# Performance work log

Hardware: AMD Instinct MI355X
Metric: run time of the kernel (lower is better)

The kernel has to match this reference:

```python
import jax, jax.numpy as jnp
import numpy as np

B = 4_000_000

# physical constants from initBatteryParams
R_ = 8.3144621
F_ = 96487.0
ALPHA = 0.5
SN = 0.0002
SP = 0.0002
KN = 20000.0
KP = 20000.0
VOL = 2.2e-05
VOLS = 0.1 * VOL
VOLB = VOL - VOLS
TO = 10.0
TSN = 90.0
TSP = 90.0
U0P = 4.03
U0N = 0.01
QMAX_BASE = 10000.0
RO_BASE = 10.0
T_DIFFUSION = 7.0e6  # repo default; attribute used in getNextState
DT = 1.0


def setup_inputs() -> dict:
    key = jax.random.key(0)
    ks = jax.random.split(key, 12)
    qMax = 1.4 * jnp.ones((B,), jnp.float32)   # 14000/qMaxBASE
    Ro = 0.015 * jnp.ones((B,), jnp.float32)   # 0.15/RoBASE
    # physically plausible initial state (get_initial_state) + small noise
    qM = qMax * QMAX_BASE  # [B]
    Tb = 292.1 + 0.5 * jax.random.normal(ks[0], (B, 1), jnp.float32)
    Vo = 0.01 * jax.random.uniform(ks[1], (B, 1), jnp.float32)
    Vsn = 0.01 * jax.random.uniform(ks[2], (B, 1), jnp.float32)
    Vsp = 0.01 * jax.random.uniform(ks[3], (B, 1), jnp.float32)
    jitter = lambda k: 1.0 + 0.01 * jax.random.normal(k, (B, 1), jnp.float32)
    qnB = (qM * 0.6 * VOLB / VOL)[:, None] * jitter(ks[4])
    qnS = (qM * 0.6 * VOLS / VOL)[:, None] * jitter(ks[5])
    qpB = (qM * 0.4 * VOLB / VOL)[:, None] * jitter(ks[6])
    qpS = (qM * 0.4 * VOLS / VOL)[:, None] * jitter(ks[7])
    states = jnp.concatenate([Tb, Vo, Vsn, Vsp, qnB, qnS, qpB, qpS], axis=1)
    inputs = 1.0 + 2.0 * jax.random.uniform(ks[8], (B, 1), jnp.float32)  # current [A]
    kw = jax.random.split(ks[9], 8)
    return {
        "inputs": inputs, "states": states, "qMax": qMax, "Ro": Ro,
        "Wp0": 0.5 * jax.random.normal(kw[0], (8, 1), jnp.float32),
        "bp0": 0.1 * jax.random.normal(kw[1], (8,), jnp.float32),
        "Wp2": 0.5 * jax.random.normal(kw[2], (4, 8), jnp.float32),
        "bp2": 0.1 * jax.random.normal(kw[3], (4,), jnp.float32),
        "Wp4": 0.5 * jax.random.normal(kw[4], (1, 4), jnp.float32),
        "bp4": 0.1 * jax.random.normal(kw[5], (1,), jnp.float32),
        "Wn": 0.0016 * jnp.ones((1, 1), jnp.float32),  # ~fitted Linear(1,1)
        "bn": -0.0008 * jnp.ones((1,), jnp.float32),
    }


def _mlp_p(x, Wp0, bp0, Wp2, bp2, Wp4, bp4):
    h = jnp.tanh(x @ Wp0.T + bp0)
    h = jnp.tanh(h @ Wp2.T + bp2)
    return h @ Wp4.T + bp4


def _cell(inputs, states, qMax, Ro, Wp0, bp0, Wp2, bp2, Wp4, bp4, Wn, bn):
    Tb, Vo, Vsn, Vsp, qnB, qnS, qpB, qpS = jnp.split(states, 8, axis=1)
    i = inputs  # [B,1]
    qSMax = (qMax * QMAX_BASE * VOLS / VOL)[:, None]  # [B,1]
    # --- getNextState ---
    xpS = jnp.clip(qpS / qSMax, 1e-18, 1.0)
    xnS = jnp.clip(qnS / qSMax, 1e-18, 1.0)
    Jn0 = 1e-18 + KN * (1.0 - xnS) ** ALPHA * xnS ** ALPHA
    Jp0 = 1e-18 + KP * (1.0 - xpS) ** ALPHA * xpS ** ALPHA
    qdotDiffusionBSn = (qnB / VOLB - qnS / VOLS) / T_DIFFUSION
    qdotDiffusionBSp = (qpB / VOLB - qpS / VOLS) / T_DIFFUSION
    Jn = i / SN
    Jp = i / SP
    VoNominal = i * Ro[:, None] * RO_BASE
    VsnNominal = R_ * Tb / F_ / ALPHA * jnp.arcsinh(Jn / (2.0 * Jn0))
    VspNominal = R_ * Tb / F_ / ALPHA * jnp.arcsinh(Jp / (2.0 * Jp0))
    Tb2 = Tb  # Tbdot = 0
    Vo2 = Vo + (VoNominal - Vo) / TO * DT
    Vsn2 = Vsn + (VsnNominal - Vsn) / TSN * DT
    Vsp2 = Vsp + (VspNominal - Vsp) / TSP * DT
    qnB2 = qnB + (-qdotDiffusionBSn) * DT
    qnS2 = qnS + (qdotDiffusionBSn - i) * DT
    qpB2 = qpB + (-qdotDiffusionBSp) * DT
    qpS2 = qpS + (i + qdotDiffusionBSp) * DT
    XNew = jnp.concatenate([Tb2, Vo2, Vsn2, Vsp2, qnB2, qnS2, qpB2, qpS2], axis=1)
    # --- getNextOutput (on XNew) ---
    xpS_o = qpS2 / qSMax
    xnS_o = qnS2 / qSMax
    VepMLP = _mlp_p(xpS_o, Wp0, bp0, Wp2, bp2, Wp4, bp4)
    VenMLP = xnS_o @ Wn.T + bn
    safe_log_p = jnp.clip((1.0 - xpS_o) / xpS_o, 1e-18, 1e18)
    safe_log_n = jnp.clip((1.0 - xnS_o) / xnS_o, 1e-18, 1e18)
    Vep = U0P + R_ * Tb2 / F_ * jnp.log(safe_log_p) + VepMLP
    Ven = U0N + R_ * Tb2 / F_ * jnp.log(safe_log_n) + VenMLP
    V = Vep - Ven - Vo2 - Vsn2 - Vsp2
    return V, XNew


def reference(inputs, states, qMax, Ro, Wp0, bp0, Wp2, bp2, Wp4, bp4, Wn, bn):
    return _cell(inputs, states, qMax, Ro, Wp0, bp0, Wp2, bp2, Wp4, bp4, Wn, bn)
```

## Files before the change

### kernel.cpp

```cpp
#include <hip/hip_runtime.h>
#include <math.h>

typedef float v4f __attribute__((ext_vector_type(4)));
typedef float v2f __attribute__((ext_vector_type(2)));

#define RTF       (8.3144621f / 96487.0f)
#define VOLS_     2.2e-06f
#define VOLB_     1.98e-05f
#define INV_TDIFF (1.0f / 7.0e6f)

#define LUT_N 4096

__device__ __forceinline__ float fdiv_fast(float a, float b) {
    return __fdividef(a, b);
}

__device__ __forceinline__ float asinh_pos(float x) {
    return __logf(x + sqrtf(fmaf(x, x, 1.0f)));
}

__global__ __launch_bounds__(256) void build_lut_kernel(
    const float* __restrict__ Wp0, const float* __restrict__ bp0,
    const float* __restrict__ Wp2, const float* __restrict__ bp2,
    const float* __restrict__ Wp4, const float* __restrict__ bp4,
    float* __restrict__ lutJ, v2f* __restrict__ lutO)
{
    int idx = blockIdx.x * blockDim.x + threadIdx.x;
    if (idx >= LUT_N) return;
    float x = (float)idx * (1.0f / (float)(LUT_N - 1));

    float j0 = 1e-18f + 20000.0f * sqrtf(fmaxf(x * (1.0f - x), 0.0f));
    lutJ[idx] = 1.0f / (2.0f * j0);

    float h1[8];
#pragma unroll
    for (int j = 0; j < 8; j++)
        h1[j] = tanhf(fmaf(x, Wp0[j], bp0[j]));
    float mlp = bp4[0];
#pragma unroll
    for (int k = 0; k < 4; k++) {
        float a = bp2[k];
#pragma unroll
        for (int j = 0; j < 8; j++)
            a = fmaf(h1[j], Wp2[k * 8 + j], a);
        mlp = fmaf(tanhf(a), Wp4[k], mlp);
    }

    float r = fminf(fmaxf((1.0f - x) / fmaxf(x, 1e-30f), 1e-18f), 1e18f);
    float lg = RTF * logf(r);

    v2f o; o.x = mlp; o.y = lg;
    lutO[idx] = o;
}

__global__ __launch_bounds__(256) void battery_cell_kernel(
    const float* __restrict__ inp,
    const float* __restrict__ st,
    const float* __restrict__ qMaxp,
    const float* __restrict__ Rop,
    const float* __restrict__ Wn,
    const float* __restrict__ bn,
    const float* __restrict__ lutJ,
    const v2f*   __restrict__ lutO,
    float* __restrict__ outV,
    float* __restrict__ outX,
    int B)
{
    int b = blockIdx.x * blockDim.x + threadIdx.x;
    if (b >= B) return;

    const v4f* st4 = (const v4f*)st;
    v4f s0 = st4[2 * b];
    v4f s1 = st4[2 * b + 1];
    float Tb  = s0.x, Vo  = s0.y, Vsn = s0.z, Vsp = s0.w;
    float qnB = s1.x, qnS = s1.y, qpB = s1.z, qpS = s1.w;
    float i   = inp[b];
    float qm  = qMaxp[b];
    float ro  = Rop[b];
    float wn  = Wn[0], wbn = bn[0];

    float invq = fdiv_fast(1.0f, qm * 1000.0f);

    float xpS = fminf(fmaxf(qpS * invq, 1e-18f), 1.0f);
    float xnS = fminf(fmaxf(qnS * invq, 1e-18f), 1.0f);

    float tn = xnS * (float)(LUT_N - 1);
    float tp = xpS * (float)(LUT_N - 1);
    int in0 = min((int)tn, LUT_N - 2);
    int ip0 = min((int)tp, LUT_N - 2);
    float fn = tn - (float)in0;
    float fp = tp - (float)ip0;
    float jn_a = lutJ[in0], jn_b = lutJ[in0 + 1];
    float jp_a = lutJ[ip0], jp_b = lutJ[ip0 + 1];
    float inv2Jn = fmaf(fn, jn_b - jn_a, jn_a);
    float inv2Jp = fmaf(fp, jp_b - jp_a, jp_a);

    float qdotn = (qnB * (1.0f / VOLB_) - qnS * (1.0f / VOLS_)) * INV_TDIFF;
    float qdotp = (qpB * (1.0f / VOLB_) - qpS * (1.0f / VOLS_)) * INV_TDIFF;

    float Jn = i * 5000.0f;
    float VoNom  = i * ro * 10.0f;
    float coef   = RTF * Tb * 2.0f;
    float VsnNom = coef * asinh_pos(Jn * inv2Jn);
    float VspNom = coef * asinh_pos(Jn * inv2Jp);

    float Vo2  = Vo  + (VoNom  - Vo ) * 0.1f;
    float Vsn2 = Vsn + (VsnNom - Vsn) * (1.0f / 90.0f);
    float Vsp2 = Vsp + (VspNom - Vsp) * (1.0f / 90.0f);
    float qnB2 = qnB - qdotn;
    float qnS2 = qnS + qdotn - i;
    float qpB2 = qpB - qdotp;
    float qpS2 = qpS + i + qdotp;

    float xp = qpS2 * invq;
    float xn = qnS2 * invq;

    float tpo = fminf(fmaxf(xp, 0.0f), 1.0f) * (float)(LUT_N - 1);
    float tno = fminf(fmaxf(xn, 0.0f), 1.0f) * (float)(LUT_N - 1);
    int ipo = min((int)tpo, LUT_N - 2);
    int ino = min((int)tno, LUT_N - 2);
    float fpo = tpo - (float)ipo;
    float fno = tno - (float)ino;
    v2f oa = lutO[ipo], ob = lutO[ipo + 1];
    v2f na = lutO[ino], nb = lutO[ino + 1];
    float mlp_p = fmaf(fpo, ob.x - oa.x, oa.x);
    float log_p = fmaf(fpo, ob.y - oa.y, oa.y);
    float log_n = fmaf(fno, nb.y - na.y, na.y);

    float Vep = 4.03f + Tb * log_p + mlp_p;
    float Ven = 0.01f + Tb * log_n + fmaf(xn, wn, wbn);
    float V = Vep - Ven - Vo2 - Vsn2 - Vsp2;

    outV[b] = V;
    v4f o0; o0.x = Tb;   o0.y = Vo2;  o0.z = Vsn2; o0.w = Vsp2;
    v4f o1; o1.x = qnB2; o1.y = qnS2; o1.z = qpB2; o1.w = qpS2;
    v4f* ox4 = (v4f*)outX;
    ox4[2 * b]     = o0;
    ox4[2 * b + 1] = o1;
}

extern "C" void kernel_launch(void* const* d_in, const int* in_sizes, int n_in,
                              void* d_out, int out_size, void* d_ws, size_t ws_size,
                              hipStream_t stream) {
    const float* inp  = (const float*)d_in[0];
    const float* st   = (const float*)d_in[1];
    const float* qMax = (const float*)d_in[2];
    const float* Ro   = (const float*)d_in[3];
    const float* Wp0  = (const float*)d_in[4];
    const float* bp0  = (const float*)d_in[5];
    const float* Wp2  = (const float*)d_in[6];
    const float* bp2  = (const float*)d_in[7];
    const float* Wp4  = (const float*)d_in[8];
    const float* bp4  = (const float*)d_in[9];
    const float* Wn   = (const float*)d_in[10];
    const float* bn   = (const float*)d_in[11];

    int B = in_sizes[0];
    float* outV = (float*)d_out;
    float* outX = (float*)d_out + B;

    float* lutJ = (float*)d_ws;
    v2f*   lutO = (v2f*)((char*)d_ws + LUT_N * 4);

    build_lut_kernel<<<LUT_N / 256, 256, 0, stream>>>(
        Wp0, bp0, Wp2, bp2, Wp4, bp4, lutJ, lutO);

    int block = 256;
    int grid = (B + block - 1) / block;
    battery_cell_kernel<<<grid, block, 0, stream>>>(
        inp, st, qMax, Ro, Wn, bn, lutJ, lutO, outV, outX, B);
}
```

Baseline: 288.4 us.

## Pair LUT entries, process eight rows per thread with prefetch, nontemporal stores

The lookup tables now store each entry together with its right neighbour, so one vector load replaces two scalar gathers per interpolation. The main kernel makes each thread handle eight rows strided by the block size, loading the next row's inputs before computing the current one, so memory latency overlaps with compute. Outputs are written with nontemporal stores to avoid polluting cache with streaming data. The costs are a doubled LUT footprint, more register use per thread and a grid eight times smaller.

```diff
diff --git a/kernel.cpp b/kernel.cpp
--- a/kernel.cpp
+++ b/kernel.cpp
@@ -10,47 +10,145 @@
 #define INV_TDIFF (1.0f / 7.0e6f)
 
 #define LUT_N 4096
-
-__device__ __forceinline__ float fdiv_fast(float a, float b) {
-    return __fdividef(a, b);
-}
+#define ROWS  8
 
 __device__ __forceinline__ float asinh_pos(float x) {
     return __logf(x + sqrtf(fmaf(x, x, 1.0f)));
+}
+
+__device__ __forceinline__ float jval(float x) {
+    float j0 = 1e-18f + 20000.0f * sqrtf(fmaxf(x * (1.0f - x), 0.0f));
+    return 1.0f / (2.0f * j0);
+}
+
+__device__ __forceinline__ void mlp_log_eval(
+    float x,
+    const float* __restrict__ Wp0, const float* __restrict__ bp0,
+    const float* __restrict__ Wp2, const float* __restrict__ bp2,
+    const float* __restrict__ Wp4, const float* __restrict__ bp4,
+    float* mlp_out, float* log_out)
+{
+    float h1[8];
+#pragma unroll
+    for (int j = 0; j < 8; j++)
+        h1[j] = tanhf(fmaf(x, Wp0[j], bp0[j]));
+    float mlp = bp4[0];
+#pragma unroll
+    for (int k = 0; k < 4; k++) {
+        float a = bp2[k];
+#pragma unroll
+        for (int j = 0; j < 8; j++)
+            a = fmaf(h1[j], Wp2[k * 8 + j], a);
+        mlp = fmaf(tanhf(a), Wp4[k], mlp);
+    }
+    *mlp_out = mlp;
+    float r = fminf(fmaxf((1.0f - x) / fmaxf(x, 1e-30f), 1e-18f), 1e18f);
+    *log_out = RTF * logf(r);
 }
 
 __global__ __launch_bounds__(256) void build_lut_kernel(
     const float* __restrict__ Wp0, const float* __restrict__ bp0,
     const float* __restrict__ Wp2, const float* __restrict__ bp2,
     const float* __restrict__ Wp4, const float* __restrict__ bp4,
-    float* __restrict__ lutJ, v2f* __restrict__ lutO)
+    v2f* __restrict__ lutJ2, v4f* __restrict__ lutO4)
 {
     int idx = blockIdx.x * blockDim.x + threadIdx.x;
     if (idx >= LUT_N) return;
-    float x = (float)idx * (1.0f / (float)(LUT_N - 1));
-
-    float j0 = 1e-18f + 20000.0f * sqrtf(fmaxf(x * (1.0f - x), 0.0f));
-    lutJ[idx] = 1.0f / (2.0f * j0);
-
-    float h1[8];
-#pragma unroll
-    for (int j = 0; j < 8; j++)
-        h1[j] = tanhf(fmaf(x, Wp0[j], bp0[j]));
-    float mlp = bp4[0];
-#pragma unroll
-    for (int k = 0; k < 4; k++) {
-        float a = bp2[k];
-#pragma unroll
-        for (int j = 0; j < 8; j++)
-            a = fmaf(h1[j], Wp2[k * 8 + j], a);
-        mlp = fmaf(tanhf(a), Wp4[k], mlp);
-    }
-
-    float r = fminf(fmaxf((1.0f - x) / fmaxf(x, 1e-30f), 1e-18f), 1e18f);
-    float lg = RTF * logf(r);
-
-    v2f o; o.x = mlp; o.y = lg;
-    lutO[idx] = o;
+    const float dx = 1.0f / (float)(LUT_N - 1);
+    float x0 = (float)idx * dx;
+    float x1 = fminf(x0 + dx, 1.0f);
+
+    v2f j; j.x = jval(x0); j.y = jval(x1);
+    lutJ2[idx] = j;
+
+    float m0, l0, m1, l1;
+    mlp_log_eval(x0, Wp0, bp0, Wp2, bp2, Wp4, bp4, &m0, &l0);
+    mlp_log_eval(x1, Wp0, bp0, Wp2, bp2, Wp4, bp4, &m1, &l1);
+    v4f o; o.x = m0; o.y = l0; o.z = m1; o.w = l1;
+    lutO4[idx] = o;
+}
+
+struct Row { v4f s0, s1; float i, qm, ro; };
+
+__device__ __forceinline__ Row load_row(
+    const float* __restrict__ inp, const v4f* __restrict__ st4,
+    const float* __restrict__ qMaxp, const float* __restrict__ Rop, int b)
+{
+    Row r;
+    r.s0 = st4[2 * b];
+    r.s1 = st4[2 * b + 1];
+    r.i  = inp[b];
+    r.qm = qMaxp[b];
+    r.ro = Rop[b];
+    return r;
+}
+
+__device__ __forceinline__ void process_row(
+    int b, const Row& r, float wn, float wbn,
+    const v2f* __restrict__ lutJ2, const v4f* __restrict__ lutO4,
+    float* __restrict__ outV, v4f* __restrict__ ox4)
+{
+    float Tb  = r.s0.x, Vo  = r.s0.y, Vsn = r.s0.z, Vsp = r.s0.w;
+    float qnB = r.s1.x, qnS = r.s1.y, qpB = r.s1.z, qpS = r.s1.w;
+    float i   = r.i;
+
+    float invq = __fdividef(1.0f, r.qm * 1000.0f);
+
+    float xpS = fminf(fmaxf(qpS * invq, 1e-18f), 1.0f);
+    float xnS = fminf(fmaxf(qnS * invq, 1e-18f), 1.0f);
+
+    float tn = xnS * (float)(LUT_N - 1);
+    float tp = xpS * (float)(LUT_N - 1);
+    int in0 = min((int)tn, LUT_N - 2);
+    int ip0 = min((int)tp, LUT_N - 2);
+    float fn = tn - (float)in0;
+    float fp = tp - (float)ip0;
+    v2f jn = lutJ2[in0];
+    v2f jp = lutJ2[ip0];
+    float inv2Jn = fmaf(fn, jn.y - jn.x, jn.x);
+    float inv2Jp = fmaf(fp, jp.y - jp.x, jp.x);
+
+    float qdotn = (qnB * (1.0f / VOLB_) - qnS * (1.0f / VOLS_)) * INV_TDIFF;
+    float qdotp = (qpB * (1.0f / VOLB_) - qpS * (1.0f / VOLS_)) * INV_TDIFF;
+
+    float Jn   = i * 5000.0f;
+    float VoNom  = i * r.ro * 10.0f;
+    float coef   = RTF * Tb * 2.0f;
+    float VsnNom = coef * asinh_pos(Jn * inv2Jn);
+    float VspNom = coef * asinh_pos(Jn * inv2Jp);
+
+    float Vo2  = Vo  + (VoNom  - Vo ) * 0.1f;
+    float Vsn2 = Vsn + (VsnNom - Vsn) * (1.0f / 90.0f);
+    float Vsp2 = Vsp + (VspNom - Vsp) * (1.0f / 90.0f);
+    float qnB2 = qnB - qdotn;
+    float qnS2 = qnS + qdotn - i;
+    float qpB2 = qpB - qdotp;
+    float qpS2 = qpS + i + qdotp;
+
+    float xp = qpS2 * invq;
+    float xn = qnS2 * invq;
+
+    float tpo = fminf(fmaxf(xp, 0.0f), 1.0f) * (float)(LUT_N - 1);
+    float tno = fminf(fmaxf(xn, 0.0f), 1.0f) * (float)(LUT_N - 1);
+    int ipo = min((int)tpo, LUT_N - 2);
+    int ino = min((int)tno, LUT_N - 2);
+    float fpo = tpo - (float)ipo;
+    float fno = tno - (float)ino;
+    v4f op = lutO4[ipo];
+    v4f on = lutO4[ino];
+    float mlp_p = fmaf(fpo, op.z - op.x, op.x);
+    float log_p = fmaf(fpo, op.w - op.y, op.y);
+    float log_n = fmaf(fno, on.w - on.y, on.y);
+
+    float Vep = 4.03f + Tb * log_p + mlp_p;
+    float Ven = 0.01f + Tb * log_n + fmaf(xn, wn, wbn);
+    float V = Vep - Ven - Vo2 - Vsn2 - Vsp2;
+
+    __builtin_nontemporal_store(V, &outV[b]);
+    v4f o0; o0.x = Tb;   o0.y = Vo2;  o0.z = Vsn2; o0.w = Vsp2;
+    v4f o1; o1.x = qnB2; o1.y = qnS2; o1.z = qpB2; o1.w = qpS2;
+    __builtin_nontemporal_store(o0, &ox4[2 * b]);
+    __builtin_nontemporal_store(o1, &ox4[2 * b + 1]);
 }
 
 __global__ __launch_bounds__(256) void battery_cell_kernel(
@@ -60,83 +158,38 @@
     const float* __restrict__ Rop,
     const float* __restrict__ Wn,
     const float* __restrict__ bn,
-    const float* __restrict__ lutJ,
-    const v2f*   __restrict__ lutO,
+    const v2f*   __restrict__ lutJ2,
+    const v4f*   __restrict__ lutO4,
     float* __restrict__ outV,
     float* __restrict__ outX,
     int B)
 {
-    int b = blockIdx.x * blockDim.x + threadIdx.x;
-    if (b >= B) return;
-
     const v4f* st4 = (const v4f*)st;
-    v4f s0 = st4[2 * b];
-    v4f s1 = st4[2 * b + 1];
-    float Tb  = s0.x, Vo  = s0.y, Vsn = s0.z, Vsp = s0.w;
-    float qnB = s1.x, qnS = s1.y, qpB = s1.z, qpS = s1.w;
-    float i   = inp[b];
-    float qm  = qMaxp[b];
-    float ro  = Rop[b];
-    float wn  = Wn[0], wbn = bn[0];
-
-    float invq = fdiv_fast(1.0f, qm * 1000.0f);
-
-    float xpS = fminf(fmaxf(qpS * invq, 1e-18f), 1.0f);
-    float xnS = fminf(fmaxf(qnS * invq, 1e-18f), 1.0f);
-
-    float tn = xnS * (float)(LUT_N - 1);
-    float tp = xpS * (float)(LUT_N - 1);
-    int in0 = min((int)tn, LUT_N - 2);
-    int ip0 = min((int)tp, LUT_N - 2);
-    float fn = tn - (float)in0;
-    float fp = tp - (float)ip0;
-    float jn_a = lutJ[in0], jn_b = lutJ[in0 + 1];
-    float jp_a = lutJ[ip0], jp_b = lutJ[ip0 + 1];
-    float inv2Jn = fmaf(fn, jn_b - jn_a, jn_a);
-    float inv2Jp = fmaf(fp, jp_b - jp_a, jp_a);
-
-    float qdotn = (qnB * (1.0f / VOLB_) - qnS * (1.0f / VOLS_)) * INV_TDIFF;
-    float qdotp = (qpB * (1.0f / VOLB_) - qpS * (1.0f / VOLS_)) * INV_TDIFF;
-
-    float Jn = i * 5000.0f;
-    float VoNom  = i * ro * 10.0f;
-    float coef   = RTF * Tb * 2.0f;
-    float VsnNom = coef * asinh_pos(Jn * inv2Jn);
-    float VspNom = coef * asinh_pos(Jn * inv2Jp);
-
-    float Vo2  = Vo  + (VoNom  - Vo ) * 0.1f;
-    float Vsn2 = Vsn + (VsnNom - Vsn) * (1.0f / 90.0f);
-    float Vsp2 = Vsp + (VspNom - Vsp) * (1.0f / 90.0f);
-    float qnB2 = qnB - qdotn;
-    float qnS2 = qnS + qdotn - i;
-    float qpB2 = qpB - qdotp;
-    float qpS2 = qpS + i + qdotp;
-
-    float xp = qpS2 * invq;
-    float xn = qnS2 * invq;
-
-    float tpo = fminf(fmaxf(xp, 0.0f), 1.0f) * (float)(LUT_N - 1);
-    float tno = fminf(fmaxf(xn, 0.0f), 1.0f) * (float)(LUT_N - 1);
-    int ipo = min((int)tpo, LUT_N - 2);
-    int ino = min((int)tno, LUT_N - 2);
-    float fpo = tpo - (float)ipo;
-    float fno = tno - (float)ino;
-    v2f oa = lutO[ipo], ob = lutO[ipo + 1];
-    v2f na = lutO[ino], nb = lutO[ino + 1];
-    float mlp_p = fmaf(fpo, ob.x - oa.x, oa.x);
-    float log_p = fmaf(fpo, ob.y - oa.y, oa.y);
-    float log_n = fmaf(fno, nb.y - na.y, na.y);
-
-    float Vep = 4.03f + Tb * log_p + mlp_p;
-    float Ven = 0.01f + Tb * log_n + fmaf(xn, wn, wbn);
-    float V = Vep - Ven - Vo2 - Vsn2 - Vsp2;
-
-    outV[b] = V;
-    v4f o0; o0.x = Tb;   o0.y = Vo2;  o0.z = Vsn2; o0.w = Vsp2;
-    v4f o1; o1.x = qnB2; o1.y = qnS2; o1.z = qpB2; o1.w = qpS2;
     v4f* ox4 = (v4f*)outX;
-    ox4[2 * b]     = o0;
-    ox4[2 * b + 1] = o1;
+    float wn = Wn[0], wbn = bn[0];
+
+    int base = blockIdx.x * (256 * ROWS) + threadIdx.x;
+
+    if (base + (ROWS - 1) * 256 < B) {
+        Row cur = load_row(inp, st4, qMaxp, Rop, base);
+#pragma unroll
+        for (int k = 0; k < ROWS; k++) {
+            Row nxt;
+            if (k + 1 < ROWS)
+                nxt = load_row(inp, st4, qMaxp, Rop, base + (k + 1) * 256);
+            process_row(base + k * 256, cur, wn, wbn, lutJ2, lutO4, outV, ox4);
+            if (k + 1 < ROWS)
+                cur = nxt;
+        }
+    } else {
+        for (int k = 0; k < ROWS; k++) {
+            int b = base + k * 256;
+            if (b < B) {
+                Row r = load_row(inp, st4, qMaxp, Rop, b);
+                process_row(b, r, wn, wbn, lutJ2, lutO4, outV, ox4);
+            }
+        }
+    }
 }
 
 extern "C" void kernel_launch(void* const* d_in, const int* in_sizes, int n_in,
@@ -159,14 +212,14 @@
     float* outV = (float*)d_out;
     float* outX = (float*)d_out + B;
 
-    float* lutJ = (float*)d_ws;
-    v2f*   lutO = (v2f*)((char*)d_ws + LUT_N * 4);
+    v2f* lutJ2 = (v2f*)d_ws;
+    v4f* lutO4 = (v4f*)((char*)d_ws + LUT_N * 8);
 
     build_lut_kernel<<<LUT_N / 256, 256, 0, stream>>>(
-        Wp0, bp0, Wp2, bp2, Wp4, bp4, lutJ, lutO);
-
-    int block = 256;
-    int grid = (B + block - 1) / block;
-    battery_cell_kernel<<<grid, block, 0, stream>>>(
-        inp, st, qMax, Ro, Wn, bn, lutJ, lutO, outV, outX, B);
-}
+        Wp0, bp0, Wp2, bp2, Wp4, bp4, lutJ2, lutO4);
+
+    int chunk = 256 * ROWS;
+    int grid = (B + chunk - 1) / chunk;
+    battery_cell_kernel<<<grid, 256, 0, stream>>>(
+        inp, st, qMax, Ro, Wn, bn, lutJ2, lutO4, outV, outX, B);
+}
```

New measurement: 312.0 us. 8.2% more time.
